# Optimization experiments

Hardware: AMD Instinct MI355X
Metric: run time of the kernel (lower is better)

## Reference

```python
import jax, jax.numpy as jnp
import numpy as np

KERNEL_MUL = 2.0
KERNEL_NUM = 5


def setup_inputs() -> dict:
    key = jax.random.key(0)
    k1, k2 = jax.random.split(key)
    N, D = 4096, 256
    source = jax.random.normal(k1, (N, D), dtype=jnp.float32)
    target = jax.random.normal(k2, (N, D), dtype=jnp.float32)
    return {"source": source, "target": target}


def _gaussian_kernel_sum(source, target):
    # total: [2N, D]
    total = jnp.concatenate([source, target], axis=0)
    n = total.shape[0]
    sq = jnp.sum(total * total, axis=1)  # [2N]
    L2 = sq[:, None] + sq[None, :] - 2.0 * (total @ total.T)  # [2N, 2N]
    # Bandwidth from detached mean of off-diagonal-normalized sum (torch uses .data)
    bandwidth = jax.lax.stop_gradient(jnp.sum(L2)) / (n * n - n)
    bandwidth = bandwidth / (KERNEL_MUL ** (KERNEL_NUM // 2))
    kernels = sum(
        jnp.exp(-L2 / (bandwidth * (KERNEL_MUL ** i))) for i in range(KERNEL_NUM)
    )
    return kernels


def reference(source, target):
    b = source.shape[0]
    K = _gaussian_kernel_sum(source, target)
    XX = jnp.mean(K[:b, :b])
    YY = jnp.mean(K[b:, b:])
    XY = jnp.mean(K[:b, b:])
    YX = jnp.mean(K[b:, :b])
    return XX + YY - XY - YX
```

## Files before the change

### kernel.cpp

```cpp
#include <hip/hip_runtime.h>


#define NROWS 8192
#define HALF  4096
#define DIM   256
#define CONVB 256
#define NTILE 2080

typedef float f32x4 __attribute__((ext_vector_type(4)));
typedef float f32x2 __attribute__((ext_vector_type(2)));

__device__ __forceinline__ const float* row_ptr(const float* src, const float* tgt, int r) {
    return (r < HALF) ? (src + (size_t)r * DIM) : (tgt + (size_t)(r - HALF) * DIM);
}

__device__ __forceinline__ void gload_lds16(const void* g, void* l) {
    __builtin_amdgcn_global_load_lds(
        (const __attribute__((address_space(1))) unsigned int*)g,
        (__attribute__((address_space(3))) unsigned int*)l, 16, 0, 0);
}

__global__ __launch_bounds__(256) void k_conv(const float* __restrict__ src,
                                              const float* __restrict__ tgt,
                                              unsigned char* __restrict__ hi,
                                              float* __restrict__ sq,
                                              float* __restrict__ part,
                                              double* __restrict__ parts1,
                                              float* __restrict__ out) {
    __shared__ __align__(16) unsigned char sh8[32 * 256];
    __shared__ float4 cs[4][64];
    __shared__ double s1s[4];

    int w = threadIdx.x >> 6, lane = threadIdx.x & 63;
    int r0 = blockIdx.x * 32;

    float4 v[8];
    #pragma unroll
    for (int i = 0; i < 8; ++i) {
        int row = r0 + w * 8 + i;
        v[i] = ((const float4*)row_ptr(src, tgt, row))[lane];
    }

    float4 csum = {0.f, 0.f, 0.f, 0.f};
    double s1w = 0.0;
    #pragma unroll
    for (int i = 0; i < 8; ++i) {
        int rl  = w * 8 + i;
        float xs[4] = {v[i].x, v[i].y, v[i].z, v[i].w};
        int pk = __builtin_amdgcn_cvt_pk_fp8_f32(xs[0], xs[1], 0, false);
        pk     = __builtin_amdgcn_cvt_pk_fp8_f32(xs[2], xs[3], pk, true);
        int o  = lane >> 1, h = lane & 1;
        *(int*)&sh8[rl * 256 + (((o ^ rl) & 31) << 3) + (h << 2)] = pk;
        csum.x += xs[0]; csum.y += xs[1]; csum.z += xs[2]; csum.w += xs[3];
        float sf = xs[0]*xs[0] + xs[1]*xs[1] + xs[2]*xs[2] + xs[3]*xs[3];
        float q0 = __builtin_amdgcn_cvt_f32_fp8(pk, 0);
        float q1 = __builtin_amdgcn_cvt_f32_fp8(pk, 1);
        float q2 = __builtin_amdgcn_cvt_f32_fp8(pk, 2);
        float q3 = __builtin_amdgcn_cvt_f32_fp8(pk, 3);
        float sQ = q0*q0 + q1*q1 + q2*q2 + q3*q3;
        #pragma unroll
        for (int off = 32; off; off >>= 1) {
            sf += __shfl_xor(sf, off, 64);
            sQ += __shfl_xor(sQ, off, 64);
        }
        if (lane == 0) { sq[r0 + rl] = sQ; s1w += (double)sf; }
    }
    __syncthreads();
    int panel = blockIdx.x >> 2, quarter = blockIdx.x & 3;
    #pragma unroll
    for (int c = threadIdx.x; c < 512; c += 256) {
        int u = c >> 5, rl = c & 31;
        int tt = u >> 2, j = u & 3;
        int o0 = 8 * tt + j;
        int o1 = 8 * tt + 4 + j;
        unsigned long long q0 = *(const unsigned long long*)
            &sh8[rl * 256 + (((o0 ^ rl) & 31) << 3)];
        unsigned long long q1 = *(const unsigned long long*)
            &sh8[rl * 256 + (((o1 ^ rl) & 31) << 3)];
        ulonglong2 q = {q0, q1};
        size_t goff = ((size_t)panel * 2048 + (size_t)u * 128 + quarter * 32 + rl);
        ((ulonglong2*)hi)[goff] = q;
    }
    cs[w][lane] = csum;
    if (lane == 0) s1s[w] = s1w;
    __syncthreads();
    if (w == 0) {
        float4 a = cs[0][lane], b = cs[1][lane], c = cs[2][lane], d = cs[3][lane];
        float4 tot = {a.x + b.x + c.x + d.x, a.y + b.y + c.y + d.y,
                      a.z + b.z + c.z + d.z, a.w + b.w + c.w + d.w};
        *(float4*)&part[(size_t)blockIdx.x * DIM + lane * 4] = tot;
        if (lane == 0) parts1[blockIdx.x] = s1s[0] + s1s[1] + s1s[2] + s1s[3];
    }
    if (blockIdx.x == 0 && threadIdx.x == 0) out[0] = 0.0f;
}

__global__ __launch_bounds__(256) void k_scale(const double* __restrict__ parts1,
                                               const float* __restrict__ part,
                                               float* __restrict__ scale) {
    __shared__ double sh[256];
    int t = threadIdx.x;
    sh[t] = parts1[t];
    __syncthreads();
    for (int off = 128; off; off >>= 1) {
        if (t < off) sh[t] += sh[t + off];
        __syncthreads();
    }
    double S1 = sh[0];
    __syncthreads();
    float c0 = 0.f, c1 = 0.f, c2 = 0.f, c3 = 0.f;
    #pragma unroll 16
    for (int b = 0; b < CONVB; b += 4) {
        c0 += part[(b + 0) * DIM + t];
        c1 += part[(b + 1) * DIM + t];
        c2 += part[(b + 2) * DIM + t];
        c3 += part[(b + 3) * DIM + t];
    }
    double c = (double)((c0 + c1) + (c2 + c3));
    sh[t] = c * c;
    __syncthreads();
    for (int off = 128; off; off >>= 1) {
        if (t < off) sh[t] += sh[t + off];
        __syncthreads();
    }
    if (t == 0) {
        double S2    = sh[0];
        double n     = (double)NROWS;
        double sumL2 = 2.0 * n * S1 - 2.0 * S2;
        double bw    = sumL2 / (n * n - n) / 4.0;
        *scale = (float)(-1.0 / (16.0 * bw * 0.69314718055994530942));
    }
}

__global__ __launch_bounds__(256, 2) void k_pairs(const unsigned char* __restrict__ hi,
                                                  const float* __restrict__ sq,
                                                  const float* __restrict__ scale_p,
                                                  float* __restrict__ pb) {
    __shared__ __align__(16) ulonglong2 ldsA[2048];
    __shared__ __align__(16) ulonglong2 ldsB[2048];
    __shared__ float wsum[4];

    int id = blockIdx.x;
    int I = 0;
    for (;;) {
        int cnt = 64 - I;
        if (id < cnt) break;
        id -= cnt; ++I;
    }
    int J = I + id;

    int t    = threadIdx.x;
    int lane = t & 63;
    int w    = t >> 6;
    int lr   = lane & 15, lq = lane >> 4;
    int wr   = w >> 1, wc = w & 1;

    float wgt = (J == I) ? 1.0f : 2.0f;
    float sgn = ((I < 32) == (J < 32)) ? 1.0f : -1.0f;

    const ulonglong2* plane = (const ulonglong2*)hi;
    int nIns = (J == I) ? 32 : 64;
    for (int i = 0; i < 16; ++i) {
        int k = w + 4 * i;
        if (k >= nIns) break;
        int p  = k >> 5;
        int u  = (k >> 1) & 15;
        int h  = k & 1;
        int rg = (h * 64 + lane) ^ ((u & 3) << 1);
        size_t gUnit = (size_t)(p ? J : I) * 2048 + (size_t)u * 128 + rg;
        ulonglong2* ldst = (p ? ldsB : ldsA) + (u * 128 + h * 64);
        gload_lds16(plane + gUnit, ldst);
    }
    asm volatile("s_waitcnt vmcnt(0)");
    __syncthreads();

    const ulonglong2* lA = ldsA;
    const ulonglong2* lB = (J == I) ? ldsA : ldsB;
    int lrx = lr ^ (lq << 1);
    const ulonglong2* pAl = lA + lq * 128 + wr * 64 + lrx;
    const ulonglong2* pBl = lB + lq * 128 + wc * 64 + lrx;

    f32x4 acc[4][4];
    #pragma unroll
    for (int m = 0; m < 4; ++m)
        #pragma unroll
        for (int n = 0; n < 4; ++n) acc[m][n] = (f32x4){0.f, 0.f, 0.f, 0.f};

    #pragma unroll
    for (int tt = 0; tt < 4; ++tt) {
        ulonglong2 fA[4], fB[4];
        #pragma unroll
        for (int m = 0; m < 4; ++m) fA[m] = pAl[tt * 512 + m * 16];
        #pragma unroll
        for (int n = 0; n < 4; ++n) fB[n] = pBl[tt * 512 + n * 16];
        #pragma unroll
        for (int m = 0; m < 4; ++m)
            #pragma unroll
            for (int n = 0; n < 4; ++n)
                acc[m][n] = __builtin_amdgcn_mfma_f32_16x16x32_fp8_fp8(
                    (long)fA[m].x, (long)fB[n].x, acc[m][n], 0, 0, 0);
        #pragma unroll
        for (int m = 0; m < 4; ++m)
            #pragma unroll
            for (int n = 0; n < 4; ++n)
                acc[m][n] = __builtin_amdgcn_mfma_f32_16x16x32_fp8_fp8(
                    (long)fA[m].y, (long)fB[n].y, acc[m][n], 0, 0, 0);
    }

    float s = *scale_p;
    int ro_eff = I * 128 + wr * 64;
    int co_eff = J * 128 + wc * 64;
    float4 sqa4[4];
    float  sqbv[4];
    #pragma unroll
    for (int m = 0; m < 4; ++m) sqa4[m] = *(const float4*)&sq[ro_eff + m * 16 + lq * 4];
    #pragma unroll
    for (int n = 0; n < 4; ++n) sqbv[n] = s * sq[co_eff + n * 16 + lr];

    f32x2 ssa01[4], ssa23[4];
    #pragma unroll
    for (int m = 0; m < 4; ++m) {
        ssa01[m] = (f32x2){s * sqa4[m].x, s * sqa4[m].y};
        ssa23[m] = (f32x2){s * sqa4[m].z, s * sqa4[m].w};
    }
    f32x2 m2s = {-2.0f * s, -2.0f * s};

    f32x2 t0 = {0.f, 0.f}, t1 = {0.f, 0.f};
    #pragma unroll
    for (int m = 0; m < 4; ++m) {
        #pragma unroll
        for (int n = 0; n < 4; ++n) {
            f32x2 sbn = {sqbv[n], sqbv[n]};
            f32x2 a01 = {acc[m][n][0], acc[m][n][1]};
            f32x2 a23 = {acc[m][n][2], acc[m][n][3]};
            f32x2 e01 = (ssa01[m] + sbn) + m2s * a01;
            f32x2 e23 = (ssa23[m] + sbn) + m2s * a23;
            f32x2 u01, u23;
            u01.x = __builtin_amdgcn_exp2f(e01.x);
            u01.y = __builtin_amdgcn_exp2f(e01.y);
            u23.x = __builtin_amdgcn_exp2f(e23.x);
            u23.y = __builtin_amdgcn_exp2f(e23.y);
            f32x2 p2a = u01 * u01, p4a = p2a * p2a, p8a = p4a * p4a, p16a = p8a * p8a;
            f32x2 p2b = u23 * u23, p4b = p2b * p2b, p8b = p4b * p4b, p16b = p8b * p8b;
            t0 += ((u01 + p2a) + (p4a + p8a)) + p16a;
            t1 += ((u23 + p2b) + (p4b + p8b)) + p16b;
        }
    }
    float tsum = (t0.x + t0.y) + (t1.x + t1.y);

    #pragma unroll
    for (int off = 32; off; off >>= 1) tsum += __shfl_xor(tsum, off, 64);
    if (lane == 0) wsum[w] = tsum;
    __syncthreads();
    if (t == 0) {
        float tot = wsum[0] + wsum[1] + wsum[2] + wsum[3];
        pb[blockIdx.x] = tot * sgn * wgt * (1.0f / ((float)HALF * (float)HALF));
    }
}

__global__ __launch_bounds__(256) void k_fin(const float* __restrict__ pb,
                                             float* __restrict__ out) {
    __shared__ float sh[4];
    int t = threadIdx.x, lane = t & 63, w = t >> 6;
    float s = 0.f;
    for (int i = t; i < NTILE; i += 256) s += pb[i];
    #pragma unroll
    for (int off = 32; off; off >>= 1) s += __shfl_xor(s, off, 64);
    if (lane == 0) sh[w] = s;
    __syncthreads();
    if (t == 0) out[0] = sh[0] + sh[1] + sh[2] + sh[3];
}

extern "C" void kernel_launch(void* const* d_in, const int* in_sizes, int n_in,
                              void* d_out, int out_size, void* d_ws, size_t ws_size,
                              hipStream_t stream) {
    const float* src = (const float*)d_in[0];
    const float* tgt = (const float*)d_in[1];
    float* out = (float*)d_out;

    char* ws = (char*)d_ws;
    float*  scale  = (float*)(ws + 16);
    float*  sq     = (float*)(ws + 64);
    float*  part   = (float*)(ws + 64 + 32768);
    double* parts1 = (double*)(ws + 64 + 32768 + 262144);
    unsigned char* hi = (unsigned char*)(ws + 297024);
    float*  pb     = (float*)(ws + 2394176);

    k_conv <<<CONVB, 256, 0, stream>>>(src, tgt, hi, sq, part, parts1, out);
    k_scale<<<1, 256, 0, stream>>>(parts1, part, scale);
    k_pairs<<<NTILE, 256, 0, stream>>>(hi, sq, scale, pb);
    k_fin  <<<1, 256, 0, stream>>>(pb, out);
}
```

Measured before the change: 97.47 us.

## Make pair kernel persistent over contiguous tile ranges with panel reuse and prefetch

The pair kernel now launches a fixed grid of 512 blocks. Each block walks a contiguous range of upper-triangular tiles in row-major order. It keeps the row panel in LDS when consecutive tiles share a row and loads only the changed panel. The next panel is prefetched asynchronously while the current tile runs its MFMA and exp work, which aims to cut redundant LDS staging and hide load latency. The cost is holding all fragments in registers across the loop, extra barriers per tile, and possible load imbalance between blocks.

```diff
diff --git a/kernel.cpp b/kernel.cpp
--- a/kernel.cpp
+++ b/kernel.cpp
@@ -6,6 +6,7 @@
 #define DIM   256
 #define CONVB 256
 #define NTILE 2080
+#define GRIDP 512
 
 typedef float f32x4 __attribute__((ext_vector_type(4)));
 typedef float f32x2 __attribute__((ext_vector_type(2)));
@@ -18,6 +19,19 @@
     __builtin_amdgcn_global_load_lds(
         (const __attribute__((address_space(1))) unsigned int*)g,
         (__attribute__((address_space(3))) unsigned int*)l, 16, 0, 0);
+}
+
+__device__ __forceinline__ void stage_panel(const ulonglong2* plane, int P,
+                                            ulonglong2* lds, int w, int lane) {
+    #pragma unroll
+    for (int i = 0; i < 8; ++i) {
+        int k = w + 4 * i;
+        int u = k >> 1;
+        int h = k & 1;
+        int rg = (h * 64 + lane) ^ ((u & 3) << 1);
+        gload_lds16(plane + (size_t)P * 2048 + (size_t)u * 128 + rg,
+                    lds + u * 128 + h * 64);
+    }
 }
 
 __global__ __launch_bounds__(256) void k_conv(const float* __restrict__ src,
@@ -139,12 +153,15 @@
     __shared__ __align__(16) ulonglong2 ldsB[2048];
     __shared__ float wsum[4];
 
-    int id = blockIdx.x;
-    int I = 0;
+    int bid = blockIdx.x;
+    int t0 = (bid * NTILE) / GRIDP;
+    int t1 = ((bid + 1) * NTILE) / GRIDP;
+
+    int id = t0, I = 0;
     for (;;) {
-        int cnt = 64 - I;
-        if (id < cnt) break;
-        id -= cnt; ++I;
+        int c = 64 - I;
+        if (id < c) break;
+        id -= c; ++I;
     }
     int J = I + id;
 
@@ -153,107 +170,117 @@
     int w    = t >> 6;
     int lr   = lane & 15, lq = lane >> 4;
     int wr   = w >> 1, wc = w & 1;
-
-    float wgt = (J == I) ? 1.0f : 2.0f;
-    float sgn = ((I < 32) == (J < 32)) ? 1.0f : -1.0f;
+    int lrx  = lr ^ (lq << 1);
 
     const ulonglong2* plane = (const ulonglong2*)hi;
-    int nIns = (J == I) ? 32 : 64;
-    for (int i = 0; i < 16; ++i) {
-        int k = w + 4 * i;
-        if (k >= nIns) break;
-        int p  = k >> 5;
-        int u  = (k >> 1) & 15;
-        int h  = k & 1;
-        int rg = (h * 64 + lane) ^ ((u & 3) << 1);
-        size_t gUnit = (size_t)(p ? J : I) * 2048 + (size_t)u * 128 + rg;
-        ulonglong2* ldst = (p ? ldsB : ldsA) + (u * 128 + h * 64);
-        gload_lds16(plane + gUnit, ldst);
-    }
+    float s = *scale_p;
+    f32x2 m2s = {-2.0f * s, -2.0f * s};
+
+    stage_panel(plane, I, ldsA, w, lane);
+    if (J != I) stage_panel(plane, J, ldsB, w, lane);
     asm volatile("s_waitcnt vmcnt(0)");
     __syncthreads();
 
-    const ulonglong2* lA = ldsA;
-    const ulonglong2* lB = (J == I) ? ldsA : ldsB;
-    int lrx = lr ^ (lq << 1);
-    const ulonglong2* pAl = lA + lq * 128 + wr * 64 + lrx;
-    const ulonglong2* pBl = lB + lq * 128 + wc * 64 + lrx;
-
-    f32x4 acc[4][4];
-    #pragma unroll
-    for (int m = 0; m < 4; ++m)
-        #pragma unroll
-        for (int n = 0; n < 4; ++n) acc[m][n] = (f32x4){0.f, 0.f, 0.f, 0.f};
-
-    #pragma unroll
-    for (int tt = 0; tt < 4; ++tt) {
-        ulonglong2 fA[4], fB[4];
-        #pragma unroll
-        for (int m = 0; m < 4; ++m) fA[m] = pAl[tt * 512 + m * 16];
-        #pragma unroll
-        for (int n = 0; n < 4; ++n) fB[n] = pBl[tt * 512 + n * 16];
+    float wtot = 0.0f;
+    int curI = I, curJ = J;
+
+    #pragma unroll 1
+    for (int tile = t0; tile < t1; ++tile) {
+        const ulonglong2* lB  = (curJ == curI) ? ldsA : ldsB;
+        const ulonglong2* pAl = ldsA + lq * 128 + wr * 64 + lrx;
+        const ulonglong2* pBl = lB   + lq * 128 + wc * 64 + lrx;
+
+        ulonglong2 fA[4][4], fB[4][4];
+        #pragma unroll
+        for (int tt = 0; tt < 4; ++tt) {
+            #pragma unroll
+            for (int m = 0; m < 4; ++m) fA[tt][m] = pAl[tt * 512 + m * 16];
+            #pragma unroll
+            for (int n = 0; n < 4; ++n) fB[tt][n] = pBl[tt * 512 + n * 16];
+        }
+        __syncthreads();
+
+        int nI = curI, nJ = curJ + 1;
+        if (nJ == 64) { nI = curI + 1; nJ = nI; }
+        if (tile + 1 < t1) {
+            if (nI != curI) stage_panel(plane, nI, ldsA, w, lane);
+            else            stage_panel(plane, nJ, ldsB, w, lane);
+        }
+
+        f32x4 acc[4][4];
         #pragma unroll
         for (int m = 0; m < 4; ++m)
             #pragma unroll
-            for (int n = 0; n < 4; ++n)
-                acc[m][n] = __builtin_amdgcn_mfma_f32_16x16x32_fp8_fp8(
-                    (long)fA[m].x, (long)fB[n].x, acc[m][n], 0, 0, 0);
-        #pragma unroll
-        for (int m = 0; m < 4; ++m)
-            #pragma unroll
-            for (int n = 0; n < 4; ++n)
-                acc[m][n] = __builtin_amdgcn_mfma_f32_16x16x32_fp8_fp8(
-                    (long)fA[m].y, (long)fB[n].y, acc[m][n], 0, 0, 0);
-    }
-
-    float s = *scale_p;
-    int ro_eff = I * 128 + wr * 64;
-    int co_eff = J * 128 + wc * 64;
-    float4 sqa4[4];
-    float  sqbv[4];
-    #pragma unroll
-    for (int m = 0; m < 4; ++m) sqa4[m] = *(const float4*)&sq[ro_eff + m * 16 + lq * 4];
-    #pragma unroll
-    for (int n = 0; n < 4; ++n) sqbv[n] = s * sq[co_eff + n * 16 + lr];
-
-    f32x2 ssa01[4], ssa23[4];
-    #pragma unroll
-    for (int m = 0; m < 4; ++m) {
-        ssa01[m] = (f32x2){s * sqa4[m].x, s * sqa4[m].y};
-        ssa23[m] = (f32x2){s * sqa4[m].z, s * sqa4[m].w};
-    }
-    f32x2 m2s = {-2.0f * s, -2.0f * s};
-
-    f32x2 t0 = {0.f, 0.f}, t1 = {0.f, 0.f};
-    #pragma unroll
-    for (int m = 0; m < 4; ++m) {
-        #pragma unroll
-        for (int n = 0; n < 4; ++n) {
-            f32x2 sbn = {sqbv[n], sqbv[n]};
-            f32x2 a01 = {acc[m][n][0], acc[m][n][1]};
-            f32x2 a23 = {acc[m][n][2], acc[m][n][3]};
-            f32x2 e01 = (ssa01[m] + sbn) + m2s * a01;
-            f32x2 e23 = (ssa23[m] + sbn) + m2s * a23;
-            f32x2 u01, u23;
-            u01.x = __builtin_amdgcn_exp2f(e01.x);
-            u01.y = __builtin_amdgcn_exp2f(e01.y);
-            u23.x = __builtin_amdgcn_exp2f(e23.x);
-            u23.y = __builtin_amdgcn_exp2f(e23.y);
-            f32x2 p2a = u01 * u01, p4a = p2a * p2a, p8a = p4a * p4a, p16a = p8a * p8a;
-            f32x2 p2b = u23 * u23, p4b = p2b * p2b, p8b = p4b * p4b, p16b = p8b * p8b;
-            t0 += ((u01 + p2a) + (p4a + p8a)) + p16a;
-            t1 += ((u23 + p2b) + (p4b + p8b)) + p16b;
-        }
-    }
-    float tsum = (t0.x + t0.y) + (t1.x + t1.y);
-
-    #pragma unroll
-    for (int off = 32; off; off >>= 1) tsum += __shfl_xor(tsum, off, 64);
-    if (lane == 0) wsum[w] = tsum;
+            for (int n = 0; n < 4; ++n) acc[m][n] = (f32x4){0.f, 0.f, 0.f, 0.f};
+        #pragma unroll
+        for (int tt = 0; tt < 4; ++tt) {
+            #pragma unroll
+            for (int m = 0; m < 4; ++m)
+                #pragma unroll
+                for (int n = 0; n < 4; ++n)
+                    acc[m][n] = __builtin_amdgcn_mfma_f32_16x16x32_fp8_fp8(
+                        (long)fA[tt][m].x, (long)fB[tt][n].x, acc[m][n], 0, 0, 0);
+            #pragma unroll
+            for (int m = 0; m < 4; ++m)
+                #pragma unroll
+                for (int n = 0; n < 4; ++n)
+                    acc[m][n] = __builtin_amdgcn_mfma_f32_16x16x32_fp8_fp8(
+                        (long)fA[tt][m].y, (long)fB[tt][n].y, acc[m][n], 0, 0, 0);
+        }
+
+        float wgt = (curJ == curI) ? 1.0f : 2.0f;
+        float sgn = ((curI < 32) == (curJ < 32)) ? 1.0f : -1.0f;
+        int ro_eff = curI * 128 + wr * 64;
+        int co_eff = curJ * 128 + wc * 64;
+        float4 sqa4[4];
+        float  sqbv[4];
+        #pragma unroll
+        for (int m = 0; m < 4; ++m) sqa4[m] = *(const float4*)&sq[ro_eff + m * 16 + lq * 4];
+        #pragma unroll
+        for (int n = 0; n < 4; ++n) sqbv[n] = s * sq[co_eff + n * 16 + lr];
+
+        f32x2 ssa01[4], ssa23[4];
+        #pragma unroll
+        for (int m = 0; m < 4; ++m) {
+            ssa01[m] = (f32x2){s * sqa4[m].x, s * sqa4[m].y};
+            ssa23[m] = (f32x2){s * sqa4[m].z, s * sqa4[m].w};
+        }
+
+        f32x2 acc0 = {0.f, 0.f}, acc1 = {0.f, 0.f};
+        #pragma unroll
+        for (int m = 0; m < 4; ++m) {
+            #pragma unroll
+            for (int n = 0; n < 4; ++n) {
+                f32x2 sbn = {sqbv[n], sqbv[n]};
+                f32x2 a01 = {acc[m][n][0], acc[m][n][1]};
+                f32x2 a23 = {acc[m][n][2], acc[m][n][3]};
+                f32x2 e01 = (ssa01[m] + sbn) + m2s * a01;
+                f32x2 e23 = (ssa23[m] + sbn) + m2s * a23;
+                f32x2 u01, u23;
+                u01.x = __builtin_amdgcn_exp2f(e01.x);
+                u01.y = __builtin_amdgcn_exp2f(e01.y);
+                u23.x = __builtin_amdgcn_exp2f(e23.x);
+                u23.y = __builtin_amdgcn_exp2f(e23.y);
+                f32x2 p2a = u01 * u01, p4a = p2a * p2a, p8a = p4a * p4a, p16a = p8a * p8a;
+                f32x2 p2b = u23 * u23, p4b = p2b * p2b, p8b = p4b * p4b, p16b = p8b * p8b;
+                acc0 += ((u01 + p2a) + (p4a + p8a)) + p16a;
+                acc1 += ((u23 + p2b) + (p4b + p8b)) + p16b;
+            }
+        }
+        wtot += ((acc0.x + acc0.y) + (acc1.x + acc1.y)) * sgn * wgt;
+
+        asm volatile("s_waitcnt vmcnt(0)");
+        __syncthreads();
+        curI = nI; curJ = nJ;
+    }
+
+    #pragma unroll
+    for (int off = 32; off; off >>= 1) wtot += __shfl_xor(wtot, off, 64);
+    if (lane == 0) wsum[w] = wtot;
     __syncthreads();
     if (t == 0) {
         float tot = wsum[0] + wsum[1] + wsum[2] + wsum[3];
-        pb[blockIdx.x] = tot * sgn * wgt * (1.0f / ((float)HALF * (float)HALF));
+        pb[blockIdx.x] = tot * (1.0f / ((float)HALF * (float)HALF));
     }
 }
 
@@ -262,7 +289,7 @@
     __shared__ float sh[4];
     int t = threadIdx.x, lane = t & 63, w = t >> 6;
     float s = 0.f;
-    for (int i = t; i < NTILE; i += 256) s += pb[i];
+    for (int i = t; i < GRIDP; i += 256) s += pb[i];
     #pragma unroll
     for (int off = 32; off; off >>= 1) s += __shfl_xor(s, off, 64);
     if (lane == 0) sh[w] = s;
@@ -287,6 +314,6 @@
 
     k_conv <<<CONVB, 256, 0, stream>>>(src, tgt, hi, sq, part, parts1, out);
     k_scale<<<1, 256, 0, stream>>>(parts1, part, scale);
-    k_pairs<<<NTILE, 256, 0, stream>>>(hi, sq, scale, pb);
+    k_pairs<<<GRIDP, 256, 0, stream>>>(hi, sq, scale, pb);
     k_fin  <<<1, 256, 0, stream>>>(pb, out);
 }
```

After: 96.35 us. About the same (-1.2%).
